# Optimization experiments

Measured on AMD Instinct MI355X. Metric: run time of the kernel, lower is better.

The kernel has to match this reference:

```python
import jax, jax.numpy as jnp
import numpy as np

N = 50000
E = 800000
IN_C, HID_C, OUT_C = 512, 128, 64


def setup_inputs() -> dict:
    key = jax.random.key(0)
    k = jax.random.split(key, 8)
    x = jax.random.normal(k[0], (N, IN_C), dtype=jnp.float32)
    edge_index = jax.random.randint(k[1], (2, E), 0, N, dtype=jnp.int64)
    edge_weight = jax.random.uniform(k[2], (E,), dtype=jnp.float32)
    # GCNConv parameters (glorot-like init)
    W1 = jax.random.normal(k[3], (IN_C, HID_C), dtype=jnp.float32) * (1.0 / np.sqrt(IN_C))
    b1 = jnp.zeros((HID_C,), dtype=jnp.float32)
    W2 = jax.random.normal(k[4], (HID_C, OUT_C), dtype=jnp.float32) * (1.0 / np.sqrt(HID_C))
    b2 = jnp.zeros((OUT_C,), dtype=jnp.float32)
    return {"x": x, "edge_index": edge_index, "edge_weight": edge_weight,
            "W1": W1, "b1": b1, "W2": W2, "b2": b2}


def _add_self_loops(edge_index, edge_weight, num_nodes):
    loop = jnp.arange(num_nodes, dtype=edge_index.dtype)
    ei = jnp.concatenate([edge_index, jnp.stack([loop, loop])], axis=1)
    ew = jnp.concatenate([edge_weight, jnp.ones((num_nodes,), edge_weight.dtype)])
    return ei, ew


def _gcn_conv(x, row, col, norm, W, b, num_nodes):
    # linear transform first (PyG GCNConv), then normalized scatter-add aggregation
    xw = x @ W                                    # [N, F_out]
    msg = norm[:, None] * xw[row]                 # gather + scale, [E', F_out]
    out = jnp.zeros((num_nodes, xw.shape[1]), xw.dtype).at[col].add(msg)
    return out + b


def reference(x, edge_index, edge_weight, W1, b1, W2, b2):
    num_nodes = x.shape[0]
    ei, ew = _add_self_loops(edge_index, edge_weight, num_nodes)
    row, col = ei[0], ei[1]
    # symmetric normalization: D^{-1/2} A D^{-1/2} (deg over destination index)
    deg = jnp.zeros((num_nodes,), ew.dtype).at[col].add(ew)
    dinv = jnp.where(deg > 0, jax.lax.rsqrt(deg), 0.0)
    norm = dinv[row] * ew * dinv[col]
    h = _gcn_conv(x, row, col, norm, W1, b1, num_nodes)
    h = jax.nn.relu(h)
    # dropout p=0.5 is identity in eval mode
    return _gcn_conv(h, row, col, norm, W2, b2, num_nodes)
```

## Files before the change

kernel.cpp:

```cpp
#include <hip/hip_runtime.h>

#define NNODES 50000
#define NEDGES 800000
#define IN_C   512
#define HID_C  128
#define OUT_C  64
#define NBUCK  196
#define BCAP   5120
#define BREG   5376

typedef float  f32x4  __attribute__((ext_vector_type(4)));
typedef __bf16 bf16x8 __attribute__((ext_vector_type(8)));
typedef short  short8 __attribute__((ext_vector_type(8)));

#define GLDS(src, dst) \
  __builtin_amdgcn_global_load_lds( \
      (const __attribute__((address_space(1))) unsigned int*)(src), \
      (__attribute__((address_space(3))) unsigned int*)(dst), 16, 0, 0)

__device__ __forceinline__ float bf2f(unsigned short u) {
  unsigned int x = (unsigned int)u << 16;
  return __builtin_bit_cast(float, x);
}
__device__ __forceinline__ unsigned short f16bits(float f) {
  _Float16 h = (_Float16)f;
  return __builtin_bit_cast(unsigned short, h);
}
__device__ __forceinline__ float f16val(unsigned short u) {
  return (float)__builtin_bit_cast(_Float16, u);
}


__device__ __forceinline__ void wsplit_one(const float* __restrict__ W,
                                           unsigned short* __restrict__ Th,
                                           unsigned short* __restrict__ Tl,
                                           int K, int N, int id) {
  int k = id % K, n = id / K;
  float f = W[(size_t)k * N + n];
  __bf16 hb = (__bf16)f;
  __bf16 lb = (__bf16)(f - (float)hb);
  Th[id] = __builtin_bit_cast(unsigned short, hb);
  Tl[id] = __builtin_bit_cast(unsigned short, lb);
}

__global__ void __launch_bounds__(256) prep0_kernel(
    unsigned int* __restrict__ gclaim,
    const float* __restrict__ W1, unsigned short* __restrict__ W1th,
    unsigned short* __restrict__ W1tl,
    const float* __restrict__ W2, unsigned short* __restrict__ W2th,
    unsigned short* __restrict__ W2tl) {
  int id = blockIdx.x * blockDim.x + threadIdx.x;
  if (id < 256) { if (id < NBUCK) gclaim[id] = (unsigned int)id * BCAP; return; }
  int s = id - 256;
  if (s < IN_C * HID_C) wsplit_one(W1, W1th, W1tl, IN_C, HID_C, s);
  else if (s < IN_C * HID_C + HID_C * OUT_C)
    wsplit_one(W2, W2th, W2tl, HID_C, OUT_C, s - IN_C * HID_C);
}

template <int K, int N, int WR, int WC>
__device__ __forceinline__ void gemm_body(const float* __restrict__ X,
                                          const unsigned short* __restrict__ Bth,
                                          const unsigned short* __restrict__ Btl,
                                          unsigned short* __restrict__ Y, int M, int bid) {
  constexpr int NW = WR * WC;
  constexpr int BM = WR * 32;
  constexpr int NI = K / 32;
  constexpr int ASLOTS = (BM / 8) / NW;
  constexpr int BSLOTS = (N / 8) / NW;

  __shared__ float          As[2][BM * 32];
  __shared__ unsigned short Bs[2][2][N * 32];

  int tid = threadIdx.x;
  int lane = tid & 63, wid = tid >> 6;
  int wr = wid / WC, wc = wid % WC;
  int row0blk = bid * BM;
  int row0 = row0blk + wr * 32;
  int rlo = lane & 15;
  int khi = lane >> 4;

  f32x4 acc[2][4] = {};

  auto stage = [&](int t, int buf) {
    int kb = t * 32;
#pragma unroll
    for (int i = 0; i < ASLOTS; ++i) {
      int slot = wid * ASLOTS + i;
      int rt = slot * 8 + (lane >> 3);
      int gr = row0blk + rt; gr = gr < M ? gr : M - 1;
      int gs = (lane & 7) ^ (lane >> 3);
      GLDS(X + (size_t)gr * K + kb + gs * 4, &As[buf][slot * 256]);
    }
#pragma unroll
    for (int i = 0; i < BSLOTS; ++i) {
      int slot = wid * BSLOTS + i;
      int half = slot / (N / 16);
      int idx = slot % (N / 16);
      const unsigned short* Wt = half ? Btl : Bth;
      int c = idx * 16 + (lane >> 2);
      int gs = (lane & 3) ^ (lane >> 4);
      GLDS(Wt + (size_t)c * K + kb + gs * 8, &Bs[buf][half][idx * 512]);
    }
  };

  stage(0, 0);
  __syncthreads();

#pragma unroll 1
  for (int t = 0; t < NI; ++t) {
    int buf = t & 1;
    if (t + 1 < NI) stage(t + 1, buf ^ 1);

    bf16x8 ah[2], al[2];
#pragma unroll
    for (int m = 0; m < 2; ++m) {
      int rt = wr * 32 + m * 16 + rlo;
      int p0 = (khi * 2) ^ (rlo & 7), p1 = (khi * 2 + 1) ^ (rlo & 7);
      f32x4 v0 = *reinterpret_cast<const f32x4*>(&As[buf][rt * 32 + p0 * 4]);
      f32x4 v1 = *reinterpret_cast<const f32x4*>(&As[buf][rt * 32 + p1 * 4]);
      float f[8] = {v0.x, v0.y, v0.z, v0.w, v1.x, v1.y, v1.z, v1.w};
#pragma unroll
      for (int i = 0; i < 8; ++i) {
        __bf16 hv = (__bf16)f[i];
        ah[m][i] = hv;
        al[m][i] = (__bf16)(f[i] - (float)hv);
      }
    }
    short8 bh[4], bl[4];
#pragma unroll
    for (int n = 0; n < 4; ++n) {
      int c = wc * 64 + n * 16 + rlo;
      int pos = khi ^ (rlo >> 2);
      bh[n] = *reinterpret_cast<const short8*>(&Bs[buf][0][c * 32 + pos * 8]);
      bl[n] = *reinterpret_cast<const short8*>(&Bs[buf][1][c * 32 + pos * 8]);
    }
#pragma unroll
    for (int m = 0; m < 2; ++m)
#pragma unroll
      for (int n = 0; n < 4; ++n)
        acc[m][n] = __builtin_amdgcn_mfma_f32_16x16x32_bf16(
            ah[m], __builtin_bit_cast(bf16x8, bh[n]), acc[m][n], 0, 0, 0);
#pragma unroll
    for (int m = 0; m < 2; ++m)
#pragma unroll
      for (int n = 0; n < 4; ++n)
        acc[m][n] = __builtin_amdgcn_mfma_f32_16x16x32_bf16(
            al[m], __builtin_bit_cast(bf16x8, bh[n]), acc[m][n], 0, 0, 0);
#pragma unroll
    for (int m = 0; m < 2; ++m)
#pragma unroll
      for (int n = 0; n < 4; ++n)
        acc[m][n] = __builtin_amdgcn_mfma_f32_16x16x32_bf16(
            ah[m], __builtin_bit_cast(bf16x8, bl[n]), acc[m][n], 0, 0, 0);
    __syncthreads();
  }

#pragma unroll
  for (int m = 0; m < 2; ++m)
#pragma unroll
    for (int j = 0; j < 4; ++j) {
      int row = row0 + m * 16 + khi * 4 + j;
      if (row < M) {
#pragma unroll
        for (int n = 0; n < 4; ++n) {
          __bf16 q = (__bf16)acc[m][n][j];
          Y[(size_t)row * N + wc * 64 + n * 16 + rlo] = __builtin_bit_cast(unsigned short, q);
        }
      }
    }
}

__global__ void __launch_bounds__(512, 4) fused_gemm1_scatter_kernel(
    const float* __restrict__ X, const unsigned short* __restrict__ Bth,
    const unsigned short* __restrict__ Btl, unsigned short* __restrict__ Y, int M,
    int ngemm, const int* __restrict__ ei, const float* __restrict__ ew,
    unsigned int* __restrict__ gclaim, unsigned long long* __restrict__ binned, int nE) {
  if ((int)blockIdx.x < ngemm) {
    gemm_body<IN_C, HID_C, 4, 2>(X, Bth, Btl, Y, M, blockIdx.x);
    return;
  }
  __shared__ unsigned int h[NBUCK];
  __shared__ unsigned int cur[NBUCK];
  int t = threadIdx.x;
  if (t < NBUCK) h[t] = 0;
  __syncthreads();
  int base = ((int)blockIdx.x - ngemm) * 4096;
  int r[8]; unsigned int c[8]; unsigned short wb[8];
#pragma unroll
  for (int i = 0; i < 8; ++i) {
    int e = base + i * 512 + t;
    if (e < nE) {
      r[i] = ei[e];
      c[i] = (unsigned int)ei[nE + e];
      wb[i] = f16bits(ew[e]);
      atomicAdd(&h[c[i] >> 8], 1u);
    } else {
      c[i] = 0xFFFFFFFFu;
    }
  }
  __syncthreads();
  if (t < NBUCK) cur[t] = h[t] ? atomicAdd(&gclaim[t], h[t]) : 0u;
  __syncthreads();
#pragma unroll
  for (int i = 0; i < 8; ++i) {
    if (c[i] != 0xFFFFFFFFu) {
      unsigned int pos = atomicAdd(&cur[c[i] >> 8], 1u);
      unsigned long long rec = (unsigned long long)((unsigned int)r[i] & 0xFFFFu)
                             | ((unsigned long long)(c[i] & 0xFFu) << 16)
                             | ((unsigned long long)wb[i] << 32);
      binned[pos] = rec;
    }
  }
}


__global__ void __launch_bounds__(256) bucket_deg_kernel(
    const unsigned long long* __restrict__ binned, const unsigned int* __restrict__ gclaim,
    float* __restrict__ dinv, int* __restrict__ offs, unsigned short* __restrict__ cnts) {
  int b = blockIdx.x, t = threadIdx.x;
  int base = b * BCAP;
  int cnt = (int)gclaim[b] - base;
  int nb = min(256, NNODES - b * 256);
  __shared__ unsigned int ec[256], wf[256];
  __shared__ int sc[256];
  ec[t] = 0; wf[t] = 0;
  __syncthreads();
  for (int i = t; i < cnt; i += 256) {
    unsigned long long rec = binned[base + i];
    int dlo = (int)((rec >> 16) & 255ULL);
    atomicAdd(&ec[dlo], 1u);
    float w = f16val((unsigned short)(rec >> 32));
    atomicAdd(&wf[dlo], (unsigned int)(w * 1048576.0f + 0.5f));
  }
  __syncthreads();
  int cn = (t < nb) ? (int)ec[t] + 1 : 0;
  sc[t] = cn;
  __syncthreads();
  for (int off = 1; off < 256; off <<= 1) {
    int u = (t >= off) ? sc[t - off] : 0;
    __syncthreads();
    sc[t] += u;
    __syncthreads();
  }
  if (t < nb) {
    float deg = (float)wf[t] * (1.0f / 1048576.0f) + 1.0f;
    int g = b * 256 + t;
    dinv[g] = rsqrtf(deg);
    offs[g] = b * BREG + sc[t] - cn;
    cnts[g] = (unsigned short)ec[t];
  }
}


__global__ void __launch_bounds__(256) bucket_fill_kernel(
    const unsigned long long* __restrict__ binned, const unsigned int* __restrict__ gclaim,
    const float* __restrict__ dinv, const int* __restrict__ offs,
    unsigned int* __restrict__ edges) {
  int b = blockIdx.x, t = threadIdx.x;
  int base = b * BCAP;
  int cnt = (int)gclaim[b] - base;
  int nb = min(256, NNODES - b * 256);
  int csrbase = b * BREG;
  __shared__ unsigned int image[BREG];
  __shared__ unsigned int cur[256];
  __shared__ float ldv[256];
  float di = 0.f;
  if (t < nb) {
    int g = b * 256 + t;
    di = dinv[g];
    int loc = offs[g] - csrbase;
    cur[t] = (unsigned int)(loc + 1);
    image[loc] = (unsigned int)g | ((unsigned int)f16bits(di * di) << 16);
  }
  ldv[t] = di;
  __syncthreads();
  for (int i = t; i < cnt; i += 256) {
    unsigned long long rec = binned[base + i];
    int src = (int)(rec & 0xFFFFULL);
    int dlo = (int)((rec >> 16) & 255ULL);
    float w = f16val((unsigned short)(rec >> 32));
    float nm = dinv[src] * w * ldv[dlo];
    unsigned int pos = atomicAdd(&cur[dlo], 1u);
    image[pos] = (unsigned int)src | ((unsigned int)f16bits(nm) << 16);
  }
  __syncthreads();
  int total = cnt + nb;
  for (int j = t; j < total; j += 256) edges[csrbase + j] = image[j];
}

template <int K, int N, int WR, int WC>
__global__ void __launch_bounds__(WR * WC * 64, 4) gemm_bf16a_kernel(
    const unsigned short* __restrict__ X, const unsigned short* __restrict__ Bth,
    const unsigned short* __restrict__ Btl, unsigned short* __restrict__ Y, int M) {
  constexpr int NW = WR * WC;
  constexpr int BM = WR * 32;
  constexpr int NI = K / 32;
  constexpr int ASLOTS = (BM / 16) / NW;
  constexpr int BSLOTS = (N / 8) / NW;

  __shared__ unsigned short As[2][BM * 32];
  __shared__ unsigned short Bs[2][2][N * 32];

  int tid = threadIdx.x;
  int lane = tid & 63, wid = tid >> 6;
  int wr = wid / WC, wc = wid % WC;
  int row0blk = blockIdx.x * BM;
  int row0 = row0blk + wr * 32;
  int rlo = lane & 15;
  int khi = lane >> 4;

  f32x4 acc[2][4] = {};

  auto stage = [&](int t, int buf) {
    int kb = t * 32;
#pragma unroll
    for (int i = 0; i < ASLOTS; ++i) {
      int slot = wid * ASLOTS + i;
      int rt = slot * 16 + (lane >> 2);
      int gr = row0blk + rt; gr = gr < M ? gr : M - 1;
      int gs = (lane & 3) ^ ((lane >> 3) & 3);
      GLDS(X + (size_t)gr * K + kb + gs * 8, &As[buf][slot * 512]);
    }
#pragma unroll
    for (int i = 0; i < BSLOTS; ++i) {
      int slot = wid * BSLOTS + i;
      int half = slot / (N / 16);
      int idx = slot % (N / 16);
      const unsigned short* Wt = half ? Btl : Bth;
      int c = idx * 16 + (lane >> 2);
      int gs = (lane & 3) ^ (lane >> 4);
      GLDS(Wt + (size_t)c * K + kb + gs * 8, &Bs[buf][half][idx * 512]);
    }
  };

  stage(0, 0);
  __syncthreads();

#pragma unroll 1
  for (int t = 0; t < NI; ++t) {
    int buf = t & 1;
    if (t + 1 < NI) stage(t + 1, buf ^ 1);

    short8 ah[2];
#pragma unroll
    for (int m = 0; m < 2; ++m) {
      int rt = wr * 32 + m * 16 + rlo;
      int g = khi ^ ((rt >> 1) & 3);
      ah[m] = *reinterpret_cast<const short8*>(&As[buf][rt * 32 + g * 8]);
    }
    short8 bh[4], bl[4];
#pragma unroll
    for (int n = 0; n < 4; ++n) {
      int c = wc * 64 + n * 16 + rlo;
      int pos = khi ^ (rlo >> 2);
      bh[n] = *reinterpret_cast<const short8*>(&Bs[buf][0][c * 32 + pos * 8]);
      bl[n] = *reinterpret_cast<const short8*>(&Bs[buf][1][c * 32 + pos * 8]);
    }
#pragma unroll
    for (int m = 0; m < 2; ++m)
#pragma unroll
      for (int n = 0; n < 4; ++n)
        acc[m][n] = __builtin_amdgcn_mfma_f32_16x16x32_bf16(
            __builtin_bit_cast(bf16x8, ah[m]), __builtin_bit_cast(bf16x8, bh[n]),
            acc[m][n], 0, 0, 0);
#pragma unroll
    for (int m = 0; m < 2; ++m)
#pragma unroll
      for (int n = 0; n < 4; ++n)
        acc[m][n] = __builtin_amdgcn_mfma_f32_16x16x32_bf16(
            __builtin_bit_cast(bf16x8, ah[m]), __builtin_bit_cast(bf16x8, bl[n]),
            acc[m][n], 0, 0, 0);
    __syncthreads();
  }

#pragma unroll
  for (int m = 0; m < 2; ++m)
#pragma unroll
    for (int j = 0; j < 4; ++j) {
      int row = row0 + m * 16 + khi * 4 + j;
      if (row < M) {
#pragma unroll
        for (int n = 0; n < 4; ++n) {
          __bf16 q = (__bf16)acc[m][n][j];
          Y[(size_t)row * N + wc * 64 + n * 16 + rlo] = __builtin_bit_cast(unsigned short, q);
        }
      }
    }
}

template <int FSLICE, int FSTRIDE, bool RELU, bool OUTBF>
__global__ void __launch_bounds__(256) agg_kernel(const unsigned short* __restrict__ feat,
                                                  const int* __restrict__ offs,
                                                  const unsigned short* __restrict__ cnts,
                                                  const unsigned int* __restrict__ edges,
                                                  const float* __restrict__ bias,
                                                  void* __restrict__ outv, int foff, int n) {
  constexpr int LPN = FSLICE / 8;
  constexpr int NPW = 64 / LPN;
  constexpr int NPB = 4 * NPW;
  int wid = threadIdx.x >> 6;
  int lane = threadIdx.x & 63;
  int node = blockIdx.x * NPB + wid * NPW + lane / LPN;
  int lf = (lane % LPN) * 8;
  if (node >= n) return;
  int e0 = offs[node];
  int e1 = e0 + 1 + (int)cnts[node];
  const unsigned short* fp = feat + foff + lf;

  float acc[8];
#pragma unroll
  for (int j = 0; j < 8; ++j) acc[j] = bias[foff + lf + j];

  auto fmaEdge = [&](unsigned int q) {
    float w = f16val((unsigned short)(q >> 16));
    int row = (int)(q & 0xFFFFu);
    short8 v = *reinterpret_cast<const short8*>(fp + (size_t)row * FSTRIDE);
#pragma unroll
    for (int j = 0; j < 8; ++j)
      acc[j] = fmaf(w, bf2f((unsigned short)v[j]), acc[j]);
  };

  int e = e0;
  for (; e + 4 <= e1; e += 4) {
    unsigned int q0 = edges[e], q1 = edges[e + 1], q2 = edges[e + 2], q3 = edges[e + 3];
    fmaEdge(q0); fmaEdge(q1); fmaEdge(q2); fmaEdge(q3);
  }
  for (; e < e1; ++e) fmaEdge(edges[e]);

  if (RELU) {
#pragma unroll
    for (int j = 0; j < 8; ++j) acc[j] = fmaxf(acc[j], 0.f);
  }
  if constexpr (OUTBF) {
    short8 o;
#pragma unroll
    for (int j = 0; j < 8; ++j) {
      __bf16 q = (__bf16)acc[j];
      o[j] = (short)__builtin_bit_cast(unsigned short, q);
    }
    *reinterpret_cast<short8*>((unsigned short*)outv + (size_t)node * FSTRIDE + foff + lf) = o;
  } else {
    float* out = (float*)outv;
    float4 o0 = make_float4(acc[0], acc[1], acc[2], acc[3]);
    float4 o1 = make_float4(acc[4], acc[5], acc[6], acc[7]);
    *reinterpret_cast<float4*>(&out[(size_t)node * FSTRIDE + foff + lf]) = o0;
    *reinterpret_cast<float4*>(&out[(size_t)node * FSTRIDE + foff + lf + 4]) = o1;
  }
}


extern "C" void kernel_launch(void* const* d_in, const int* in_sizes, int n_in,
                              void* d_out, int out_size, void* d_ws, size_t ws_size,
                              hipStream_t stream) {
  const float* x  = (const float*)d_in[0];
  const int*   ei = (const int*)d_in[1];
  const float* ew = (const float*)d_in[2];
  const float* W1 = (const float*)d_in[3];
  const float* b1 = (const float*)d_in[4];
  const float* W2 = (const float*)d_in[5];
  const float* b2 = (const float*)d_in[6];
  float* out = (float*)d_out;

  const int N = NNODES, E = NEDGES;

  char* p = (char*)d_ws;
  auto alloc = [&](size_t bytes) { char* r = p; p += (bytes + 255) & ~(size_t)255; return r; };
  unsigned int* gclaim = (unsigned int*)alloc(256 * 4);
  float* dinv   = (float*)alloc((size_t)N * 4);
  int*   offs   = (int*)  alloc((size_t)N * 4);
  unsigned short* cnts = (unsigned short*)alloc((size_t)N * 2);
  unsigned long long* binned = (unsigned long long*)alloc((size_t)NBUCK * BCAP * 8);
  unsigned int* edges  = (unsigned int*)alloc((size_t)NBUCK * BREG * 4);
  unsigned short* xw = (unsigned short*)alloc((size_t)N * HID_C * 2);
  unsigned short* h  = (unsigned short*)alloc((size_t)N * HID_C * 2);
  unsigned short* W1th = (unsigned short*)alloc((size_t)IN_C * HID_C * 2);
  unsigned short* W1tl = (unsigned short*)alloc((size_t)IN_C * HID_C * 2);
  unsigned short* W2th = (unsigned short*)alloc((size_t)HID_C * OUT_C * 2);
  unsigned short* W2tl = (unsigned short*)alloc((size_t)HID_C * OUT_C * 2);

  const int PREP0 = 256 + IN_C * HID_C + HID_C * OUT_C;
  prep0_kernel<<<(PREP0 + 255) / 256, 256, 0, stream>>>(
      gclaim, W1, W1th, W1tl, W2, W2th, W2tl);

  const int NGEMM = (N + 127) / 128;
  const int NSCAT = (E + 4095) / 4096;
  fused_gemm1_scatter_kernel<<<NGEMM + NSCAT, 512, 0, stream>>>(
      x, W1th, W1tl, xw, N, NGEMM, ei, ew, gclaim, binned, E);

  bucket_deg_kernel<<<NBUCK, 256, 0, stream>>>(binned, gclaim, dinv, offs, cnts);
  bucket_fill_kernel<<<NBUCK, 256, 0, stream>>>(binned, gclaim, dinv, offs, edges);

  agg_kernel<HID_C, HID_C, true, true><<<(N + 15) / 16, 256, 0, stream>>>(
      xw, offs, cnts, edges, b1, h, 0, N);

  gemm_bf16a_kernel<HID_C, OUT_C, 8, 1><<<(N + 255) / 256, 512, 0, stream>>>(h, W2th, W2tl, xw, N);
  agg_kernel<OUT_C, OUT_C, false, false><<<(N + 31) / 32, 256, 0, stream>>>(
      xw, offs, cnts, edges, b2, out, 0, N);
}
```

Measured before the change: 107.3 us.

## Merge bucket degree and fill kernels; apply dinv normalization inside aggregation

Folds the degree computation and CSR fill into one per-bucket kernel, so each bucket's binned records are reused while the block is resident and one launch is dropped. The per-edge normalization no longer needs the global dinv, so edges now store the raw fp16 weight (self-loop weight 1.0). The aggregation kernel multiplies each edge weight by dinv[src] at gather time and scales the sum by dinv[dst] before adding the bias. The cost is an extra dinv gather per edge in both aggregation passes.

```diff
diff --git a/kernel.cpp b/kernel.cpp
--- a/kernel.cpp
+++ b/kernel.cpp
@@ -214,15 +214,18 @@
 }
 
 
-__global__ void __launch_bounds__(256) bucket_deg_kernel(
+__global__ void __launch_bounds__(256) bucket_build_kernel(
     const unsigned long long* __restrict__ binned, const unsigned int* __restrict__ gclaim,
-    float* __restrict__ dinv, int* __restrict__ offs, unsigned short* __restrict__ cnts) {
+    float* __restrict__ dinv, int* __restrict__ offs, unsigned short* __restrict__ cnts,
+    unsigned int* __restrict__ edges) {
   int b = blockIdx.x, t = threadIdx.x;
   int base = b * BCAP;
   int cnt = (int)gclaim[b] - base;
   int nb = min(256, NNODES - b * 256);
-  __shared__ unsigned int ec[256], wf[256];
+  int csrbase = b * BREG;
+  __shared__ unsigned int ec[256], wf[256], cur[256];
   __shared__ int sc[256];
+  __shared__ unsigned int image[BREG];
   ec[t] = 0; wf[t] = 0;
   __syncthreads();
   for (int i = t; i < cnt; i += 256) {
@@ -245,43 +248,22 @@
   if (t < nb) {
     float deg = (float)wf[t] * (1.0f / 1048576.0f) + 1.0f;
     int g = b * 256 + t;
-    dinv[g] = rsqrtf(deg);
-    offs[g] = b * BREG + sc[t] - cn;
+    float di = rsqrtf(deg);
+    dinv[g] = di;
+    int loc = sc[t] - cn;
+    offs[g] = csrbase + loc;
     cnts[g] = (unsigned short)ec[t];
-  }
-}
-
-
-__global__ void __launch_bounds__(256) bucket_fill_kernel(
-    const unsigned long long* __restrict__ binned, const unsigned int* __restrict__ gclaim,
-    const float* __restrict__ dinv, const int* __restrict__ offs,
-    unsigned int* __restrict__ edges) {
-  int b = blockIdx.x, t = threadIdx.x;
-  int base = b * BCAP;
-  int cnt = (int)gclaim[b] - base;
-  int nb = min(256, NNODES - b * 256);
-  int csrbase = b * BREG;
-  __shared__ unsigned int image[BREG];
-  __shared__ unsigned int cur[256];
-  __shared__ float ldv[256];
-  float di = 0.f;
-  if (t < nb) {
-    int g = b * 256 + t;
-    di = dinv[g];
-    int loc = offs[g] - csrbase;
     cur[t] = (unsigned int)(loc + 1);
-    image[loc] = (unsigned int)g | ((unsigned int)f16bits(di * di) << 16);
-  }
-  ldv[t] = di;
+    image[loc] = (unsigned int)g | (0x3C00u << 16);
+  }
   __syncthreads();
   for (int i = t; i < cnt; i += 256) {
     unsigned long long rec = binned[base + i];
     int src = (int)(rec & 0xFFFFULL);
     int dlo = (int)((rec >> 16) & 255ULL);
-    float w = f16val((unsigned short)(rec >> 32));
-    float nm = dinv[src] * w * ldv[dlo];
+    unsigned int wb = (unsigned int)((rec >> 32) & 0xFFFFULL);
     unsigned int pos = atomicAdd(&cur[dlo], 1u);
-    image[pos] = (unsigned int)src | ((unsigned int)f16bits(nm) << 16);
+    image[pos] = (unsigned int)src | (wb << 16);
   }
   __syncthreads();
   int total = cnt + nb;
@@ -388,14 +370,15 @@
     }
 }
 
-template <int FSLICE, int FSTRIDE, bool RELU, bool OUTBF>
+template <int F, bool RELU, bool OUTBF>
 __global__ void __launch_bounds__(256) agg_kernel(const unsigned short* __restrict__ feat,
                                                   const int* __restrict__ offs,
                                                   const unsigned short* __restrict__ cnts,
                                                   const unsigned int* __restrict__ edges,
+                                                  const float* __restrict__ dinv,
                                                   const float* __restrict__ bias,
-                                                  void* __restrict__ outv, int foff, int n) {
-  constexpr int LPN = FSLICE / 8;
+                                                  void* __restrict__ outv, int n) {
+  constexpr int LPN = F / 8;
   constexpr int NPW = 64 / LPN;
   constexpr int NPB = 4 * NPW;
   int wid = threadIdx.x >> 6;
@@ -405,16 +388,13 @@
   if (node >= n) return;
   int e0 = offs[node];
   int e1 = e0 + 1 + (int)cnts[node];
-  const unsigned short* fp = feat + foff + lf;
-
-  float acc[8];
-#pragma unroll
-  for (int j = 0; j < 8; ++j) acc[j] = bias[foff + lf + j];
+
+  float acc[8] = {};
 
   auto fmaEdge = [&](unsigned int q) {
-    float w = f16val((unsigned short)(q >> 16));
     int row = (int)(q & 0xFFFFu);
-    short8 v = *reinterpret_cast<const short8*>(fp + (size_t)row * FSTRIDE);
+    float w = f16val((unsigned short)(q >> 16)) * dinv[row];
+    short8 v = *reinterpret_cast<const short8*>(&feat[(size_t)row * F + lf]);
 #pragma unroll
     for (int j = 0; j < 8; ++j)
       acc[j] = fmaf(w, bf2f((unsigned short)v[j]), acc[j]);
@@ -427,9 +407,11 @@
   }
   for (; e < e1; ++e) fmaEdge(edges[e]);
 
-  if (RELU) {
-#pragma unroll
-    for (int j = 0; j < 8; ++j) acc[j] = fmaxf(acc[j], 0.f);
+  float dd = dinv[node];
+#pragma unroll
+  for (int j = 0; j < 8; ++j) {
+    acc[j] = fmaf(acc[j], dd, bias[lf + j]);
+    if (RELU) acc[j] = fmaxf(acc[j], 0.f);
   }
   if constexpr (OUTBF) {
     short8 o;
@@ -438,13 +420,13 @@
       __bf16 q = (__bf16)acc[j];
       o[j] = (short)__builtin_bit_cast(unsigned short, q);
     }
-    *reinterpret_cast<short8*>((unsigned short*)outv + (size_t)node * FSTRIDE + foff + lf) = o;
+    *reinterpret_cast<short8*>((unsigned short*)outv + (size_t)node * F + lf) = o;
   } else {
     float* out = (float*)outv;
     float4 o0 = make_float4(acc[0], acc[1], acc[2], acc[3]);
     float4 o1 = make_float4(acc[4], acc[5], acc[6], acc[7]);
-    *reinterpret_cast<float4*>(&out[(size_t)node * FSTRIDE + foff + lf]) = o0;
-    *reinterpret_cast<float4*>(&out[(size_t)node * FSTRIDE + foff + lf + 4]) = o1;
+    *reinterpret_cast<float4*>(&out[(size_t)node * F + lf]) = o0;
+    *reinterpret_cast<float4*>(&out[(size_t)node * F + lf + 4]) = o1;
   }
 }
 
@@ -487,13 +469,12 @@
   fused_gemm1_scatter_kernel<<<NGEMM + NSCAT, 512, 0, stream>>>(
       x, W1th, W1tl, xw, N, NGEMM, ei, ew, gclaim, binned, E);
 
-  bucket_deg_kernel<<<NBUCK, 256, 0, stream>>>(binned, gclaim, dinv, offs, cnts);
-  bucket_fill_kernel<<<NBUCK, 256, 0, stream>>>(binned, gclaim, dinv, offs, edges);
-
-  agg_kernel<HID_C, HID_C, true, true><<<(N + 15) / 16, 256, 0, stream>>>(
-      xw, offs, cnts, edges, b1, h, 0, N);
+  bucket_build_kernel<<<NBUCK, 256, 0, stream>>>(binned, gclaim, dinv, offs, cnts, edges);
+
+  agg_kernel<HID_C, true, true><<<(N + 15) / 16, 256, 0, stream>>>(
+      xw, offs, cnts, edges, dinv, b1, h, N);
 
   gemm_bf16a_kernel<HID_C, OUT_C, 8, 1><<<(N + 255) / 256, 512, 0, stream>>>(h, W2th, W2tl, xw, N);
-  agg_kernel<OUT_C, OUT_C, false, false><<<(N + 31) / 32, 256, 0, stream>>>(
-      xw, offs, cnts, edges, b2, out, 0, N);
-}
+  agg_kernel<OUT_C, false, false><<<(N + 31) / 32, 256, 0, stream>>>(
+      xw, offs, cnts, edges, dinv, b2, out, N);
+}
```

Measured after the change: 106.8 us. Within noise of the previous version (-0.5%).
